# Kernel optimization log

Measured on AMD Instinct MI355X. Metric: run time of the kernel, lower is better.

Reference implementation:

```python
import jax, jax.numpy as jnp
import numpy as np

BSZ, P, D, C = 16, 4096, 256, 512


def setup_inputs() -> dict:
    key = jax.random.key(0)
    k1, k2 = jax.random.split(key)
    x = jax.random.normal(k1, (BSZ, P, D), dtype=jnp.float32)
    kernels = jax.random.normal(k2, (C, D), dtype=jnp.float32) * 0.001
    return {"x": x, "kernels": kernels}


def reference(x, kernels):
    bsz, Pn, d = x.shape
    # (bsz, P, C) projection scores, ReLU'd
    scores = jax.nn.relu(jnp.einsum('bpd,cd->bpc', x, kernels))
    # per-channel argmax over positions -> (bsz, C)
    idx = jnp.argmax(scores, axis=1)
    # scatter_add each kernel row into its winning position
    b_idx = jnp.arange(bsz)[:, None]  # (bsz, 1) broadcast against (bsz, C)
    src = jnp.broadcast_to(kernels, (bsz,) + kernels.shape)  # (bsz, C, d)
    out = jnp.zeros((bsz, Pn, d), dtype=x.dtype).at[b_idx, idx].add(src)
    return out
```

## Files before the change

### kernel.cpp

```cpp
#include <hip/hip_runtime.h>
#include <cstddef>
#include <cstdint>

#define BSZ 16
#define PN  4096
#define DD  256
#define CC  512
#define TP  128
#define TC  64
#define NPT (PN / TP)
#define NCT (CC / TC)
#define NKC 8

typedef short bf16x8 __attribute__((ext_vector_type(8)));
typedef float f32x4  __attribute__((ext_vector_type(4)));

#define MEMFENCE() __asm__ __volatile__("" ::: "memory")
#define WAITCNT_VM0 0x1F70

struct Top2 { float v1, v2; int i1, i2; };

__device__ __forceinline__ void t2_insert(Top2& t, float v, int i) {
  if (v > t.v1 || (v == t.v1 && i < t.i1)) {
    t.v2 = t.v1; t.i2 = t.i1; t.v1 = v; t.i1 = i;
  } else if (v > t.v2 || (v == t.v2 && i < t.i2)) {
    t.v2 = v; t.i2 = i;
  }
}

__device__ __forceinline__ void split4(float4 v, uint2& hp, uint2& lp) {
  uint32_t u0 = __float_as_uint(v.x), u1 = __float_as_uint(v.y),
           u2 = __float_as_uint(v.z), u3 = __float_as_uint(v.w);
  float l0 = v.x - __uint_as_float(u0 & 0xffff0000u);
  float l1 = v.y - __uint_as_float(u1 & 0xffff0000u);
  float l2 = v.z - __uint_as_float(u2 & 0xffff0000u);
  float l3 = v.w - __uint_as_float(u3 & 0xffff0000u);
  hp.x = __builtin_amdgcn_perm(u1, u0, 0x07060302u);
  hp.y = __builtin_amdgcn_perm(u3, u2, 0x07060302u);
  lp.x = __builtin_amdgcn_perm(__float_as_uint(l1), __float_as_uint(l0), 0x07060302u);
  lp.y = __builtin_amdgcn_perm(__float_as_uint(l3), __float_as_uint(l2), 0x07060302u);
}

__device__ __forceinline__ void gld16(const void* gsrc, void* ldst) {
  __builtin_amdgcn_global_load_lds(
      (const __attribute__((address_space(1))) unsigned int*)gsrc,
      (__attribute__((address_space(3))) unsigned int*)ldst, 16, 0, 0);
}

__global__ __launch_bounds__(256) void convert_k_kernel(
    const float* __restrict__ kern, uint32_t* __restrict__ ks) {
  const int kc = blockIdx.x, ct = blockIdx.y;
  const size_t chunk = ((size_t)ct * NKC + kc) * 4096;
#pragma unroll
  for (int s0 = 0; s0 < 2; s0++) {
    int s  = threadIdx.x + s0 * 256;
    int fp = s >> 6, kg = (s >> 4) & 3, lr = s & 15;
    int r  = fp * 16 + lr, k0 = kg * 8;
    const float* src = kern + ((size_t)ct * 128 + r) * DD + kc * 32 + k0;
    float4 v0 = *(const float4*)src, v1 = *(const float4*)(src + 4);
    uint2 h0, l0, h1, l1; split4(v0, h0, l0); split4(v1, h1, l1);
    *(uint4*)&ks[chunk + (size_t)s * 4]        = make_uint4(h0.x, h0.y, h1.x, h1.y);
    *(uint4*)&ks[chunk + 2048 + (size_t)s * 4] = make_uint4(l0.x, l0.y, l1.x, l1.y);
  }
}

__global__ __launch_bounds__(256) void score_kernel(
    const float* __restrict__ x, const uint32_t* __restrict__ ks,
    float2* __restrict__ pv2, uint32_t* __restrict__ pix) {

  __shared__ __align__(16) char lds[49152];

  const int d  = blockIdx.x;
  const int L  = (d & 7) * 512 + (d >> 3);
  const int ct = L & 7;
  const int pt = (L >> 3) & 31;
  const int b  = L >> 8;

  const int tid = threadIdx.x;
  const int lane = tid & 63, w = tid >> 6;

  const char* xbase = (const char*)(x + ((size_t)b * PN + (size_t)pt * TP) * DD);
  const int sfp = (tid >> 7) & 1, sh = (tid >> 6) & 1, sl = tid & 63;
  const int rowb = sfp * 16 + (sl & 15);
  const int koff = (sl >> 4) * 32 + sh * 16;
  const char* asrc[4];
#pragma unroll
  for (int i = 0; i < 4; i++)
    asrc[i] = xbase + (size_t)(i * 32 + rowb) * (DD * 4) + koff;

  const char* ksbase = (const char*)ks + (size_t)(ct >> 1) * NKC * 16384 + (ct & 1) * 4096;
  const char* bsrc[2];
  bsrc[0] = ksbase + tid * 16;
  bsrc[1] = ksbase + 8192 + tid * 16;

  f32x4 acc[2][4];
#pragma unroll
  for (int i = 0; i < 2; i++)
#pragma unroll
    for (int j = 0; j < 4; j++) acc[i][j] = (f32x4)0.f;

  auto issue = [&](int kc) {
    char* Ab = lds + (kc & 1) * 16384;
    char* Bb = lds + 32768 + (kc & 1) * 8192;
#pragma unroll
    for (int i = 0; i < 4; i++)
      gld16(asrc[i] + kc * 128, Ab + i * 4096 + tid * 16);
#pragma unroll
    for (int i = 0; i < 2; i++)
      gld16(bsrc[i] + kc * 16384, Bb + i * 4096 + tid * 16);
  };

  issue(0);
  for (int kc = 0; kc < NKC; kc++) {
    MEMFENCE();
    __builtin_amdgcn_s_waitcnt(WAITCNT_VM0);
    __builtin_amdgcn_s_barrier();
    MEMFENCE();
    if (kc + 1 < NKC) issue(kc + 1);

    const char* Ab = lds + (kc & 1) * 16384;
    const char* Bb = lds + 32768 + (kc & 1) * 8192;

    bf16x8 Ah[2], Al[2];
#pragma unroll
    for (int fp = 0; fp < 2; fp++) {
      float4 v0 = *(const float4*)(Ab + w * 4096 + fp * 2048 + lane * 16);
      float4 v1 = *(const float4*)(Ab + w * 4096 + fp * 2048 + 1024 + lane * 16);
      uint2 h0, l0, h1, l1; split4(v0, h0, l0); split4(v1, h1, l1);
      uint4 hh = make_uint4(h0.x, h0.y, h1.x, h1.y);
      uint4 ll = make_uint4(l0.x, l0.y, l1.x, l1.y);
      Ah[fp] = *(bf16x8*)&hh;
      Al[fp] = *(bf16x8*)&ll;
    }
#pragma unroll
    for (int fc = 0; fc < 4; fc++) {
      bf16x8 Bh = *(const bf16x8*)(Bb + fc * 1024 + lane * 16);
      bf16x8 Bl = *(const bf16x8*)(Bb + 4096 + fc * 1024 + lane * 16);
#pragma unroll
      for (int fp = 0; fp < 2; fp++) {
        acc[fp][fc] = __builtin_amdgcn_mfma_f32_16x16x32_bf16(Ah[fp], Bh, acc[fp][fc], 0, 0, 0);
        acc[fp][fc] = __builtin_amdgcn_mfma_f32_16x16x32_bf16(Ah[fp], Bl, acc[fp][fc], 0, 0, 0);
        acc[fp][fc] = __builtin_amdgcn_mfma_f32_16x16x32_bf16(Al[fp], Bh, acc[fp][fc], 0, 0, 0);
      }
    }
    MEMFENCE();
  }

  const int lr = lane & 15, kg = lane >> 4;
  float4* scratch = (float4*)lds;
  const int slot = w * 4 + kg;
#pragma unroll
  for (int fc = 0; fc < 4; fc++) {
    Top2 t; t.v1 = -1.f; t.v2 = -1.f; t.i1 = 0x7fffffff; t.i2 = 0x7fffffff;
#pragma unroll
    for (int fp = 0; fp < 2; fp++)
#pragma unroll
      for (int r = 0; r < 4; r++) {
        float v = acc[fp][fc][r]; v = v > 0.f ? v : 0.f;
        t2_insert(t, v, w * 32 + fp * 16 + kg * 4 + r);
      }
    scratch[slot * TC + fc * 16 + lr] =
        make_float4(t.v1, __int_as_float(t.i1), t.v2, __int_as_float(t.i2));
  }
  __syncthreads();

  if (tid < TC) {
    Top2 t; t.v1 = -1.f; t.v2 = -1.f; t.i1 = 0x7fffffff; t.i2 = 0x7fffffff;
#pragma unroll
    for (int s = 0; s < 16; s++) {
      float4 e = scratch[s * TC + tid];
      t2_insert(t, e.x, __float_as_int(e.y));
      t2_insert(t, e.z, __float_as_int(e.w));
    }
    int c = ct * TC + tid;
    size_t o = ((size_t)b * CC + c) * NPT + pt;
    uint32_t p1 = (uint32_t)(pt * TP + t.i1);
    uint32_t p2 = (uint32_t)(pt * TP + t.i2);
    pv2[o] = make_float2(t.v1, t.v2);
    pix[o] = (p1 << 16) | (p2 & 0xffffu);
  }
}

__global__ __launch_bounds__(64) void reduce_winner_kernel(
    const float2* __restrict__ pv2, const uint32_t* __restrict__ pix,
    const float* __restrict__ x, const float* __restrict__ kern,
    int* __restrict__ winner) {
  const int c = blockIdx.x, b = blockIdx.y;
  const int l = threadIdx.x;

  Top2 t; t.v1 = -1.f; t.v2 = -1.f; t.i1 = 0x7fffffff; t.i2 = 0x7fffffff;
  if (l < NPT) {
    size_t o = ((size_t)b * CC + c) * NPT + l;
    float2 v = pv2[o]; uint32_t ii = pix[o];
    t.v1 = v.x; t.v2 = v.y; t.i1 = (int)(ii >> 16); t.i2 = (int)(ii & 0xffffu);
  }
#pragma unroll
  for (int m = 1; m < 64; m <<= 1) {
    float uv1 = __shfl_xor(t.v1, m, 64);
    int   ui1 = __shfl_xor(t.i1, m, 64);
    float uv2 = __shfl_xor(t.v2, m, 64);
    int   ui2 = __shfl_xor(t.i2, m, 64);
    t2_insert(t, uv1, ui1);
    t2_insert(t, uv2, ui2);
  }

  int win = t.i1;
  if (t.v1 - t.v2 <= 1e-4f * t.v1 + 1e-5f) {
    const float4* x1 = (const float4*)(x + ((size_t)b * PN + t.i1) * DD);
    const float4* x2 = (const float4*)(x + ((size_t)b * PN + t.i2) * DD);
    const float4* kc = (const float4*)(kern + (size_t)c * DD);
    float4 a1 = x1[l], a2 = x2[l], k4 = kc[l];
    float s1 = a1.x * k4.x + a1.y * k4.y + a1.z * k4.z + a1.w * k4.w;
    float s2 = a2.x * k4.x + a2.y * k4.y + a2.z * k4.z + a2.w * k4.w;
#pragma unroll
    for (int m = 1; m < 64; m <<= 1) {
      s1 += __shfl_xor(s1, m, 64);
      s2 += __shfl_xor(s2, m, 64);
    }
    s1 = fmaxf(s1, 0.f); s2 = fmaxf(s2, 0.f);
    if (s2 > s1 || (s2 == s1 && t.i2 < t.i1)) win = t.i2;
  }
  if (l == 0) winner[(size_t)b * CC + c] = win;
}

__global__ __launch_bounds__(256) void write_out_kernel(
    const int* __restrict__ winner, const float* __restrict__ kern,
    float4* __restrict__ out) {
  __shared__ __align__(16) int wrow[CC];
  const int b = blockIdx.y;
  const int tid = threadIdx.x, lane = tid & 63, w = tid >> 6;
  const int p = blockIdx.x * 4 + w;

  *(int2*)&wrow[tid * 2] = *(const int2*)&winner[(size_t)b * CC + tid * 2];
  __syncthreads();

  int4 w0 = *(const int4*)&wrow[lane * 8];
  int4 w1 = *(const int4*)&wrow[lane * 8 + 4];
  int wv[8] = {w0.x, w0.y, w0.z, w0.w, w1.x, w1.y, w1.z, w1.w};

  float4 acc = make_float4(0.f, 0.f, 0.f, 0.f);
#pragma unroll
  for (int j = 0; j < 8; j++) {
    unsigned long long m = __ballot(wv[j] == p);
    while (m) {
      int bit = __ffsll((long long)m) - 1; m &= m - 1;
      int c = bit * 8 + j;
      float4 kv = ((const float4*)(kern + (size_t)c * DD))[lane];
      acc.x += kv.x; acc.y += kv.y; acc.z += kv.z; acc.w += kv.w;
    }
  }
  out[((size_t)b * PN + p) * 64 + lane] = acc;
}

extern "C" void kernel_launch(void* const* d_in, const int* in_sizes, int n_in,
                              void* d_out, int out_size, void* d_ws, size_t ws_size,
                              hipStream_t stream) {
  const float* x    = (const float*)d_in[0];
  const float* kern = (const float*)d_in[1];
  float* out = (float*)d_out;

  char* ws = (char*)d_ws;
  float2*   pv2 = (float2*)ws;
  uint32_t* pix = (uint32_t*)(ws + (size_t)BSZ * CC * NPT * sizeof(float2));
  uint32_t* ks  = (uint32_t*)(ws + 3u * 1024 * 1024);
  int*      win = (int*)(ws + 3u * 1024 * 1024 + 512u * 1024);

  convert_k_kernel<<<dim3(NKC, CC / 128), 256, 0, stream>>>(kern, ks);

  score_kernel<<<dim3(NCT * NPT * BSZ), 256, 0, stream>>>(x, ks, pv2, pix);

  reduce_winner_kernel<<<dim3(CC, BSZ), 64, 0, stream>>>(pv2, pix, x, kern, win);

  write_out_kernel<<<dim3(PN / 4, BSZ), 256, 0, stream>>>(win, kern, (float4*)out);
}
```

Measured before the change: 209.9 us.

## Preload whole kernel tile into LDS and stream x directly to registers

The score kernel now loads the entire B (kernel hi/lo bf16) tile for all K chunks into 64KB of LDS up front. The x tile is no longer staged through LDS: each wave loads its own rows directly into registers, double-buffered across K steps. This removes the per-iteration barrier and waitcnt so MFMA work can overlap global loads. It adds launch_bounds(256,2) for occupancy, in exchange for larger LDS use and more register pressure from the A prefetch buffers.

```diff
diff --git a/kernel.cpp b/kernel.cpp
--- a/kernel.cpp
+++ b/kernel.cpp
@@ -64,11 +64,11 @@
   }
 }
 
-__global__ __launch_bounds__(256) void score_kernel(
+__global__ __launch_bounds__(256, 2) void score_kernel(
     const float* __restrict__ x, const uint32_t* __restrict__ ks,
     float2* __restrict__ pv2, uint32_t* __restrict__ pix) {
 
-  __shared__ __align__(16) char lds[49152];
+  __shared__ __align__(16) char lds[65536];
 
   const int d  = blockIdx.x;
   const int L  = (d & 7) * 512 + (d >> 3);
@@ -78,20 +78,39 @@
 
   const int tid = threadIdx.x;
   const int lane = tid & 63, w = tid >> 6;
+  const int lr = lane & 15, kg = lane >> 4;
+
+  const char* ksbase = (const char*)ks + (size_t)(ct >> 1) * NKC * 16384 + (ct & 1) * 4096;
+#pragma unroll
+  for (int kc = 0; kc < NKC; kc++) {
+#pragma unroll
+    for (int h = 0; h < 2; h++)
+      gld16(ksbase + kc * 16384 + h * 8192 + tid * 16,
+            lds + kc * 8192 + h * 4096 + tid * 16);
+  }
 
   const char* xbase = (const char*)(x + ((size_t)b * PN + (size_t)pt * TP) * DD);
-  const int sfp = (tid >> 7) & 1, sh = (tid >> 6) & 1, sl = tid & 63;
-  const int rowb = sfp * 16 + (sl & 15);
-  const int koff = (sl >> 4) * 32 + sh * 16;
-  const char* asrc[4];
-#pragma unroll
-  for (int i = 0; i < 4; i++)
-    asrc[i] = xbase + (size_t)(i * 32 + rowb) * (DD * 4) + koff;
-
-  const char* ksbase = (const char*)ks + (size_t)(ct >> 1) * NKC * 16384 + (ct & 1) * 4096;
-  const char* bsrc[2];
-  bsrc[0] = ksbase + tid * 16;
-  bsrc[1] = ksbase + 8192 + tid * 16;
+  const char* ap[2][2];
+#pragma unroll
+  for (int fp = 0; fp < 2; fp++)
+#pragma unroll
+    for (int h = 0; h < 2; h++)
+      ap[fp][h] = xbase + (size_t)(w * 32 + fp * 16 + lr) * (DD * 4) + kg * 32 + h * 16;
+
+  float4 abuf[2][2][2];
+  auto loadA = [&](int kc) {
+#pragma unroll
+    for (int fp = 0; fp < 2; fp++)
+#pragma unroll
+      for (int h = 0; h < 2; h++)
+        abuf[kc & 1][fp][h] = *(const float4*)(ap[fp][h] + kc * 128);
+  };
+
+  loadA(0);
+  MEMFENCE();
+  __builtin_amdgcn_s_waitcnt(WAITCNT_VM0);
+  __builtin_amdgcn_s_barrier();
+  MEMFENCE();
 
   f32x4 acc[2][4];
 #pragma unroll
@@ -99,34 +118,16 @@
 #pragma unroll
     for (int j = 0; j < 4; j++) acc[i][j] = (f32x4)0.f;
 
-  auto issue = [&](int kc) {
-    char* Ab = lds + (kc & 1) * 16384;
-    char* Bb = lds + 32768 + (kc & 1) * 8192;
-#pragma unroll
-    for (int i = 0; i < 4; i++)
-      gld16(asrc[i] + kc * 128, Ab + i * 4096 + tid * 16);
-#pragma unroll
-    for (int i = 0; i < 2; i++)
-      gld16(bsrc[i] + kc * 16384, Bb + i * 4096 + tid * 16);
-  };
-
-  issue(0);
+#pragma unroll
   for (int kc = 0; kc < NKC; kc++) {
-    MEMFENCE();
-    __builtin_amdgcn_s_waitcnt(WAITCNT_VM0);
-    __builtin_amdgcn_s_barrier();
-    MEMFENCE();
-    if (kc + 1 < NKC) issue(kc + 1);
-
-    const char* Ab = lds + (kc & 1) * 16384;
-    const char* Bb = lds + 32768 + (kc & 1) * 8192;
+    if (kc + 1 < NKC) loadA(kc + 1);
 
     bf16x8 Ah[2], Al[2];
 #pragma unroll
     for (int fp = 0; fp < 2; fp++) {
-      float4 v0 = *(const float4*)(Ab + w * 4096 + fp * 2048 + lane * 16);
-      float4 v1 = *(const float4*)(Ab + w * 4096 + fp * 2048 + 1024 + lane * 16);
-      uint2 h0, l0, h1, l1; split4(v0, h0, l0); split4(v1, h1, l1);
+      uint2 h0, l0, h1, l1;
+      split4(abuf[kc & 1][fp][0], h0, l0);
+      split4(abuf[kc & 1][fp][1], h1, l1);
       uint4 hh = make_uint4(h0.x, h0.y, h1.x, h1.y);
       uint4 ll = make_uint4(l0.x, l0.y, l1.x, l1.y);
       Ah[fp] = *(bf16x8*)&hh;
@@ -134,8 +135,8 @@
     }
 #pragma unroll
     for (int fc = 0; fc < 4; fc++) {
-      bf16x8 Bh = *(const bf16x8*)(Bb + fc * 1024 + lane * 16);
-      bf16x8 Bl = *(const bf16x8*)(Bb + 4096 + fc * 1024 + lane * 16);
+      bf16x8 Bh = *(const bf16x8*)(lds + kc * 8192 + fc * 1024 + lane * 16);
+      bf16x8 Bl = *(const bf16x8*)(lds + kc * 8192 + 4096 + fc * 1024 + lane * 16);
 #pragma unroll
       for (int fp = 0; fp < 2; fp++) {
         acc[fp][fc] = __builtin_amdgcn_mfma_f32_16x16x32_bf16(Ah[fp], Bh, acc[fp][fc], 0, 0, 0);
@@ -143,10 +144,10 @@
         acc[fp][fc] = __builtin_amdgcn_mfma_f32_16x16x32_bf16(Al[fp], Bh, acc[fp][fc], 0, 0, 0);
       }
     }
-    MEMFENCE();
-  }
-
-  const int lr = lane & 15, kg = lane >> 4;
+  }
+
+  __syncthreads();
+
   float4* scratch = (float4*)lds;
   const int slot = w * 4 + kg;
 #pragma unroll
```

New measurement: 236.6 us. +12.7%, slower.
